# Kernel optimization log

Measured on AMD Instinct MI355X. Metric: run time of the kernel, lower is better.

Reference implementation:

```python
import jax, jax.numpy as jnp
import numpy as np

N_NODES = 20000
N_EDGES = 160000
N_GRAPHS = 64
X_DIM = 9
E_DIM = 1
U_RAW = 4096
U_DIM = 256
E_HID = 1024
E_OUT = 512
N_HID = 512
N_OUT = 1


def _lin_params(k, fan_in, fan_out):
    kw, kb = jax.random.split(k)
    bound = 1.0 / np.sqrt(fan_in)
    W = jax.random.uniform(kw, (fan_in, fan_out), jnp.float32, -bound, bound)
    b = jax.random.uniform(kb, (fan_out,), jnp.float32, -bound, bound)
    return W, b


def setup_inputs() -> dict:
    key = jax.random.key(0)
    ks = jax.random.split(key, 16)
    x = jax.random.normal(ks[0], (N_NODES, X_DIM), jnp.float32)
    edge_attr = jax.random.normal(ks[1], (N_EDGES, E_DIM), jnp.float32)
    u = jax.random.normal(ks[2], (N_GRAPHS, U_RAW), jnp.float32)
    edge_index = jax.random.randint(ks[3], (2, N_EDGES), 0, N_NODES, jnp.int64)
    batch = jax.random.randint(ks[4], (N_NODES,), 0, N_GRAPHS, jnp.int64)

    Wsel, bsel = _lin_params(ks[5], U_RAW, U_DIM)
    e_in = E_DIM + 2 * X_DIM + U_DIM  # 275
    eW1, eb1 = _lin_params(ks[6], e_in, E_HID)
    eW2, eb2 = _lin_params(ks[7], E_HID, E_HID)
    eW3, eb3 = _lin_params(ks[8], E_HID, E_HID)
    eW4, eb4 = _lin_params(ks[9], E_HID, E_HID)
    eW5, eb5 = _lin_params(ks[10], E_HID, E_OUT)
    n1W1, n1b1 = _lin_params(ks[11], E_OUT + X_DIM, N_HID)  # 521
    n1W2, n1b2 = _lin_params(ks[12], N_HID, N_HID)
    n2W1, n2b1 = _lin_params(ks[13], X_DIM + N_HID + U_DIM, N_HID)  # 777
    n2W2, n2b2 = _lin_params(ks[14], N_HID, N_OUT)

    return dict(x=x, edge_attr=edge_attr, u=u, edge_index=edge_index, batch=batch,
                Wsel=Wsel, bsel=bsel,
                eW1=eW1, eb1=eb1, eW2=eW2, eb2=eb2, eW3=eW3, eb3=eb3,
                eW4=eW4, eb4=eb4, eW5=eW5, eb5=eb5,
                n1W1=n1W1, n1b1=n1b1, n1W2=n1W2, n1b2=n1b2,
                n2W1=n2W1, n2b1=n2b1, n2W2=n2W2, n2b2=n2b2)


def _forward(x, edge_attr, u, edge_index, batch,
             Wsel, bsel, eW1, eb1, eW2, eb2, eW3, eb3, eW4, eb4, eW5, eb5,
             n1W1, n1b1, n1W2, n1b2, n2W1, n2b1, n2W2, n2b2):
    relu = jax.nn.relu
    u2 = u @ Wsel + bsel  # [B, 256]
    row, col = edge_index[0], edge_index[1]

    # EdgeModel: cat([src, dest, edge_attr, u[batch[row]]]) -> 5-layer MLP
    e = jnp.concatenate([x[row], x[col], edge_attr, u2[batch[row]]], axis=1)
    e = relu(e @ eW1 + eb1)
    e = relu(e @ eW2 + eb2)
    e = relu(e @ eW3 + eb3)
    e = relu(e @ eW4 + eb4)
    e = e @ eW5 + eb5  # [E, 512]

    # NodeModel: gather x[col], MLP1, scatter_mean over row, MLP2
    h = jnp.concatenate([x[col], e], axis=1)
    h = relu(h @ n1W1 + n1b1)
    h = relu(h @ n1W2 + n1b2)  # [E, 512]
    ssum = jax.ops.segment_sum(h, row, num_segments=x.shape[0])
    cnt = jax.ops.segment_sum(jnp.ones((h.shape[0],), h.dtype), row, num_segments=x.shape[0])
    agg = ssum / jnp.maximum(cnt, 1.0)[:, None]  # scatter_mean

    z = jnp.concatenate([x, agg, u2[batch]], axis=1)
    z = relu(z @ n2W1 + n2b1)
    z = z @ n2W2 + n2b2  # [N, 1]
    return jnp.squeeze(z)


def reference(x, edge_attr, u, edge_index, batch,
              Wsel, bsel, eW1, eb1, eW2, eb2, eW3, eb3, eW4, eb4, eW5, eb5,
              n1W1, n1b1, n1W2, n1b2, n2W1, n2b1, n2W2, n2b2):
    return _forward(x, edge_attr, u, edge_index, batch,
                    Wsel, bsel, eW1, eb1, eW2, eb2, eW3, eb3, eW4, eb4, eW5, eb5,
                    n1W1, n1b1, n1W2, n1b2, n2W1, n2b1, n2W2, n2b2)
```

## Files before the change

kernel.cpp:

```cpp
#include <hip/hip_runtime.h>

typedef _Float16 f16;
typedef __attribute__((ext_vector_type(8))) _Float16 f16x8;
typedef __attribute__((ext_vector_type(4))) float f32x4;

#define E_TOTAL 160000
#define NN 20000
#define NGRAPH 64

__device__ __forceinline__ void gl_lds16(const void* g, void* l) {
    __builtin_amdgcn_global_load_lds((const __attribute__((address_space(1))) void*)g,
                                     (__attribute__((address_space(3))) void*)l, 16, 0, 0);
}

template <int RELU, int AUXU, int AUXX, int SCAT>
__global__ __launch_bounds__(512, 2) void hgemm2(
    int M, int N, int K,
    const f16* __restrict__ A, int lda,
    const f16* __restrict__ Bt,
    f16* __restrict__ C, int ldc,
    const float* __restrict__ bias,
    const f16* __restrict__ utab, const int* __restrict__ uidx,
    const float* __restrict__ x9, const int* __restrict__ xidx, const float* __restrict__ W9,
    float* __restrict__ sout, const int* __restrict__ sidx)
{
    __shared__ __align__(16) char Ash[2][32768];
    __shared__ __align__(16) char Bsh[2][32768];
    __shared__ float Ws9[AUXX ? 2304 : 1];

    const int tid  = threadIdx.x;
    const int lane = tid & 63;
    const int w    = tid >> 6;
    const int bm = blockIdx.y * 256;
    const int bn = blockIdx.x * 256;
    const int wm = (w >> 2) * 128;
    const int wn = (w & 3) * 64;
    const int fr = lane & 15;
    const int kq = lane >> 4;

    const char* Ab = (const char*)A;
    const char* Bb = (const char*)Bt;
    const size_t lda2 = (size_t)lda * 2;
    const size_t ldb2 = (size_t)K * 2;

    f32x4 acc[8][4] = {};

    size_t offA[4], offB[4];
    int ldsoff[4];
#pragma unroll
    for (int i = 0; i < 4; ++i) {
        int cch = w * 4 + i;
        int L = cch * 1024 + lane * 16;
        int row = L >> 7;
        int scb = (L & 127) ^ ((row & 7) << 4);
        offA[i] = (size_t)(bm + row) * lda2 + scb;
        offB[i] = (size_t)(bn + row) * ldb2 + scb;
        ldsoff[i] = cch * 1024;
    }

    const int NT = K >> 6;

#pragma unroll
    for (int i = 0; i < 4; ++i) gl_lds16(Ab + offA[i], Ash[0] + ldsoff[i]);
#pragma unroll
    for (int i = 0; i < 4; ++i) gl_lds16(Bb + offB[i], Bsh[0] + ldsoff[i]);

    int cur = 0;
    for (int t = 0; t < NT; ++t) {
        if (t + 1 < NT) {
            size_t kb = (size_t)(t + 1) << 7;
#pragma unroll
            for (int i = 0; i < 4; ++i) gl_lds16(Ab + offA[i] + kb, Ash[cur ^ 1] + ldsoff[i]);
#pragma unroll
            for (int i = 0; i < 4; ++i) gl_lds16(Bb + offB[i] + kb, Bsh[cur ^ 1] + ldsoff[i]);
            asm volatile("s_waitcnt vmcnt(8)" ::: "memory");
        } else {
            asm volatile("s_waitcnt vmcnt(0)" ::: "memory");
        }
        __builtin_amdgcn_s_barrier();
        __builtin_amdgcn_sched_barrier(0);

        const char* As = Ash[cur];
        const char* Bs = Bsh[cur];

        f16x8 bv[2][4];
#pragma unroll
        for (int ks = 0; ks < 2; ++ks) {
            const int cb = (ks * 32 + kq * 8) * 2;
#pragma unroll
            for (int ni = 0; ni < 4; ++ni) {
                int r = wn + ni * 16 + fr;
                bv[ks][ni] = *(const f16x8*)(Bs + r * 128 + (cb ^ ((r & 7) << 4)));
            }
        }
        __builtin_amdgcn_s_setprio(1);
#pragma unroll
        for (int mi = 0; mi < 8; ++mi) {
            int r = wm + mi * 16 + fr;
            int sw = (r & 7) << 4;
            f16x8 a0 = *(const f16x8*)(As + r * 128 + ((kq * 16) ^ sw));
            f16x8 a1 = *(const f16x8*)(As + r * 128 + ((64 + kq * 16) ^ sw));
#pragma unroll
            for (int ni = 0; ni < 4; ++ni)
                acc[mi][ni] = __builtin_amdgcn_mfma_f32_16x16x32_f16(a0, bv[0][ni], acc[mi][ni], 0, 0, 0);
#pragma unroll
            for (int ni = 0; ni < 4; ++ni)
                acc[mi][ni] = __builtin_amdgcn_mfma_f32_16x16x32_f16(a1, bv[1][ni], acc[mi][ni], 0, 0, 0);
        }
        __builtin_amdgcn_s_setprio(0);
        __builtin_amdgcn_s_barrier();
        cur ^= 1;
    }

    if (AUXX) {
        for (int i = tid; i < 9 * 256; i += 512)
            Ws9[i] = W9[(size_t)(i >> 8) * N + bn + (i & 255)];
        __syncthreads();
    }

#pragma unroll
    for (int mi = 0; mi < 8; ++mi) {
        int r0 = bm + wm + mi * 16 + kq * 4;
#pragma unroll
        for (int r = 0; r < 4; ++r) {
            int grow = r0 + r;
            if (grow >= M) continue;
            int ub = 0;
            if (AUXU) ub = uidx[grow];
            int sb = 0;
            if (SCAT) sb = sidx[grow];
            float xv[9];
            if (AUXX) {
                int xi = xidx ? xidx[grow] : grow;
#pragma unroll
                for (int q = 0; q < 9; ++q) xv[q] = x9[(size_t)xi * 9 + q];
            }
#pragma unroll
            for (int ni = 0; ni < 4; ++ni) {
                int lcol = wn + ni * 16 + fr;
                int col = bn + lcol;
                float v = acc[mi][ni][r] + bias[col];
                if (AUXU) v += (float)utab[(size_t)ub * N + col];
                if (AUXX) {
                    float s = 0.f;
#pragma unroll
                    for (int q = 0; q < 9; ++q) s = fmaf(xv[q], Ws9[q * 256 + lcol], s);
                    v += s;
                }
                if (RELU) v = fmaxf(v, 0.f);
                if (SCAT) {
                    atomicAdd(sout + (size_t)sb * N + col, v);
                } else {
                    C[(size_t)grow * ldc + col] = (f16)v;
                }
            }
        }
    }
}

__global__ void k_wt(const float* __restrict__ W, f16* __restrict__ Wt,
                     int r0, int Ksub, int N, int Kp)
{
    size_t t = (size_t)blockIdx.x * 256 + threadIdx.x;
    if (t >= (size_t)N * Kp) return;
    int n = (int)(t / Kp), k = (int)(t % Kp);
    Wt[t] = (k < Ksub) ? (f16)W[(size_t)(r0 + k) * N + n] : (f16)0.f;
}

__global__ void k_cvt(const float* __restrict__ W, f16* __restrict__ Wt, int n)
{
    int t = blockIdx.x * 256 + threadIdx.x;
    if (t < n) Wt[t] = (f16)W[t];
}

__global__ void k_cbias(const float* __restrict__ n1W1, const float* __restrict__ eb5,
                        const float* __restrict__ n1b1, float* __restrict__ cb)
{
    int b = blockIdx.x * 256 + threadIdx.x;
    if (b >= 512) return;
    float s = n1b1[b];
    for (int c = 0; c < 512; ++c) s = fmaf(eb5[c], n1W1[(size_t)(9 + c) * 512 + b], s);
    cb[b] = s;
}

__global__ __launch_bounds__(256) void k_u2(const float* __restrict__ u,
                                            const float* __restrict__ Wsel,
                                            const float* __restrict__ bsel,
                                            f16* __restrict__ u2h)
{
    __shared__ float us[4096];
    __shared__ float red[4][64];
    const int g = blockIdx.y;
    const int c0 = blockIdx.x * 64;
    const int col = threadIdx.x & 63;
    const int kp = threadIdx.x >> 6;
    for (int i = threadIdx.x; i < 4096; i += 256) us[i] = u[(size_t)g * 4096 + i];
    __syncthreads();
    float acc = 0.f;
    for (int k = kp * 1024; k < kp * 1024 + 1024; ++k)
        acc = fmaf(us[k], Wsel[(size_t)k * 256 + c0 + col], acc);
    red[kp][col] = acc;
    __syncthreads();
    if (kp == 0) {
        float v = red[0][col] + red[1][col] + red[2][col] + red[3][col] + bsel[c0 + col];
        u2h[(size_t)g * 256 + c0 + col] = (f16)v;
    }
}

__global__ void k_gather19(int e0, int Ce,
                           const float* __restrict__ x, const float* __restrict__ eattr,
                           const int* __restrict__ ei, const int* __restrict__ batch,
                           f16* __restrict__ feat, int* __restrict__ ebat)
{
    size_t t = (size_t)blockIdx.x * 256 + threadIdx.x;
    if (t >= (size_t)Ce * 64) return;
    int i = (int)(t >> 6), j = (int)(t & 63);
    int e = e0 + i;
    float v = 0.f;
    if (j < 9)        v = x[ei[e] * 9 + j];
    else if (j < 18)  v = x[ei[E_TOTAL + e] * 9 + (j - 9)];
    else if (j == 18) v = eattr[e];
    else if (j == 19) ebat[i] = batch[ei[e]];
    feat[t] = (f16)v;
}

__global__ void k_cnt(const int* __restrict__ ei, float* __restrict__ cnt)
{
    int t = blockIdx.x * 256 + threadIdx.x;
    if (t < E_TOTAL) atomicAdd(cnt + ei[t], 1.0f);
}

__global__ void k_agg(const float* __restrict__ ssum, const float* __restrict__ cnt,
                      f16* __restrict__ agg)
{
    size_t t = (size_t)blockIdx.x * 256 + threadIdx.x;
    if (t >= (size_t)NN * 512) return;
    int n = (int)(t >> 9);
    agg[t] = (f16)(ssum[t] / fmaxf(cnt[n], 1.f));
}

__global__ void k_final(const f16* __restrict__ z1, const float* __restrict__ W,
                        const float* __restrict__ b, float* __restrict__ out)
{
    int gt = blockIdx.x * 256 + threadIdx.x;
    int row = gt >> 6;
    int lane = threadIdx.x & 63;
    if (row >= NN) return;
    float s = 0.f;
#pragma unroll
    for (int c = lane; c < 512; c += 64) s += (float)z1[(size_t)row * 512 + c] * W[c];
#pragma unroll
    for (int off = 32; off; off >>= 1) s += __shfl_down(s, off);
    if (lane == 0) out[row] = s + b[0];
}


extern "C" void kernel_launch(void* const* d_in, const int* in_sizes, int n_in,
                              void* d_out, int out_size, void* d_ws, size_t ws_size,
                              hipStream_t stream)
{
    const float* x     = (const float*)d_in[0];
    const float* eattr = (const float*)d_in[1];
    const float* u     = (const float*)d_in[2];
    const int*   ei    = (const int*)d_in[3];
    const int*   batch = (const int*)d_in[4];
    const float* Wsel  = (const float*)d_in[5];
    const float* bsel  = (const float*)d_in[6];
    const float* eW1 = (const float*)d_in[7],  * eb1 = (const float*)d_in[8];
    const float* eW2 = (const float*)d_in[9],  * eb2 = (const float*)d_in[10];
    const float* eW3 = (const float*)d_in[11], * eb3 = (const float*)d_in[12];
    const float* eW4 = (const float*)d_in[13], * eb4 = (const float*)d_in[14];
    const float* eW5 = (const float*)d_in[15], * eb5 = (const float*)d_in[16];
    const float* n1W1 = (const float*)d_in[17], * n1b1 = (const float*)d_in[18];
    const float* n1W2 = (const float*)d_in[19], * n1b2 = (const float*)d_in[20];
    const float* n2W1 = (const float*)d_in[21], * n2b1 = (const float*)d_in[22];
    const float* n2W2 = (const float*)d_in[23], * n2b2 = (const float*)d_in[24];
    float* out = (float*)d_out;

    char* ws = (char*)d_ws;
    size_t off = 0;
    auto alc = [&](size_t bytes) { char* p = ws + off; off += (bytes + 255) & ~(size_t)255; return p; };

    float* ssum  = (float*)alc((size_t)NN * 512 * 4);
    float* cnt   = (float*)alc((size_t)NN * 4);
    float* zbias = (float*)alc(1024 * 4);
    float* cbias = (float*)alc(512 * 4);
    f16* u2h     = (f16*)alc((size_t)256 * 256 * 2);
    f16* ubias_e = (f16*)alc((size_t)64 * 1024 * 2);
    f16* ubias_n = (f16*)alc((size_t)64 * 512 * 2);
    f16* eW1t19  = (f16*)alc((size_t)1024 * 64 * 2);
    f16* eW1ut   = (f16*)alc((size_t)1024 * 256 * 2);
    f16* eW2t    = (f16*)alc((size_t)1024 * 1024 * 2);
    f16* eW3t    = (f16*)alc((size_t)1024 * 1024 * 2);
    f16* eW4t    = (f16*)alc((size_t)1024 * 1024 * 2);
    f16* eW5h    = (f16*)alc((size_t)1024 * 512 * 2);
    f16* combo_t = (f16*)alc((size_t)512 * 1024 * 2);
    f16* n1W1et  = (f16*)alc((size_t)512 * 512 * 2);
    f16* n1W2t   = (f16*)alc((size_t)512 * 512 * 2);
    f16* n2W1et  = (f16*)alc((size_t)512 * 512 * 2);
    f16* n2W1ut  = (f16*)alc((size_t)512 * 256 * 2);
    f16* agg     = (f16*)alc((size_t)20224 * 512 * 2);
    f16* z1      = (f16*)alc((size_t)20224 * 512 * 2);
    size_t fixed = off;

    size_t per_edge = 64 * 2 + 1024 * 2 + 1024 * 2 + 4;
    size_t avail = ws_size > fixed ? ws_size - fixed : 0;
    long long Cmax = (long long)(avail / per_edge);
    int C;
    if (Cmax >= E_TOTAL)      C = E_TOTAL;
    else if (Cmax >= 16384)   C = (int)((Cmax / 16384) * 16384);
    else                      C = (int)((Cmax / 256) * 256);
    if (C < 256) C = 256;

    f16* featc = (f16*)(ws + fixed);
    f16* buf1  = featc + (size_t)C * 64;
    f16* buf2  = buf1 + (size_t)C * 1024;
    int* ebat  = (int*)(buf2 + (size_t)C * 1024);

    size_t zlen = (size_t)((char*)zbias - (char*)ssum) + 1024 * 4;
    hipMemsetAsync(ssum, 0, zlen, stream);

    auto wt = [&](const float* W, f16* Wt, int r0, int Ksub, int N, int Kp) {
        size_t tot = (size_t)N * Kp;
        k_wt<<<(unsigned)((tot + 255) / 256), 256, 0, stream>>>(W, Wt, r0, Ksub, N, Kp);
    };
    wt(eW1, eW1t19, 0, 19, 1024, 64);
    wt(eW1, eW1ut, 19, 256, 1024, 256);
    wt(eW2, eW2t, 0, 1024, 1024, 1024);
    wt(eW3, eW3t, 0, 1024, 1024, 1024);
    wt(eW4, eW4t, 0, 1024, 1024, 1024);
    wt(n1W1, n1W1et, 9, 512, 512, 512);
    wt(n1W2, n1W2t, 0, 512, 512, 512);
    wt(n2W1, n2W1et, 9, 512, 512, 512);
    wt(n2W1, n2W1ut, 521, 256, 512, 256);
    k_cvt<<<(1024 * 512 + 255) / 256, 256, 0, stream>>>(eW5, eW5h, 1024 * 512);

    k_u2<<<dim3(4, NGRAPH), 256, 0, stream>>>(u, Wsel, bsel, u2h);
    k_cnt<<<(E_TOTAL + 255) / 256, 256, 0, stream>>>(ei, cnt);
    k_cbias<<<2, 256, 0, stream>>>(n1W1, eb5, n1b1, cbias);

    hgemm2<0,0,0,0><<<dim3(4, 1), 512, 0, stream>>>(64, 1024, 256, u2h, 256, eW1ut,
        ubias_e, 1024, eb1, nullptr, nullptr, nullptr, nullptr, nullptr, nullptr, nullptr);
    hgemm2<0,0,0,0><<<dim3(2, 1), 512, 0, stream>>>(64, 512, 256, u2h, 256, n2W1ut,
        ubias_n, 512, n2b1, nullptr, nullptr, nullptr, nullptr, nullptr, nullptr, nullptr);

    hgemm2<0,0,0,0><<<dim3(4, 2), 512, 0, stream>>>(512, 1024, 512, n1W1et, 512, eW5h,
        combo_t, 1024, zbias, nullptr, nullptr, nullptr, nullptr, nullptr, nullptr, nullptr);

    for (int e0 = 0; e0 < E_TOTAL; e0 += C) {
        int Ce = E_TOTAL - e0 < C ? E_TOTAL - e0 : C;
        int gy = (Ce + 255) / 256;

        k_gather19<<<(unsigned)(((size_t)Ce * 64 + 255) / 256), 256, 0, stream>>>(
            e0, Ce, x, eattr, ei, batch, featc, ebat);

        hgemm2<1,1,0,0><<<dim3(4, gy), 512, 0, stream>>>(Ce, 1024, 64, featc, 64, eW1t19,
            buf1, 1024, zbias, ubias_e, ebat, nullptr, nullptr, nullptr, nullptr, nullptr);
        hgemm2<1,0,0,0><<<dim3(4, gy), 512, 0, stream>>>(Ce, 1024, 1024, buf1, 1024, eW2t,
            buf2, 1024, eb2, nullptr, nullptr, nullptr, nullptr, nullptr, nullptr, nullptr);
        hgemm2<1,0,0,0><<<dim3(4, gy), 512, 0, stream>>>(Ce, 1024, 1024, buf2, 1024, eW3t,
            buf1, 1024, eb3, nullptr, nullptr, nullptr, nullptr, nullptr, nullptr, nullptr);
        hgemm2<1,0,0,0><<<dim3(4, gy), 512, 0, stream>>>(Ce, 1024, 1024, buf1, 1024, eW4t,
            buf2, 1024, eb4, nullptr, nullptr, nullptr, nullptr, nullptr, nullptr, nullptr);

        hgemm2<1,0,1,0><<<dim3(2, gy), 512, 0, stream>>>(Ce, 512, 1024, buf2, 1024, combo_t,
            buf1, 512, cbias, nullptr, nullptr, x, ei + E_TOTAL + e0, n1W1, nullptr, nullptr);

        hgemm2<1,0,0,1><<<dim3(2, gy), 512, 0, stream>>>(Ce, 512, 512, buf1, 512, n1W2t,
            nullptr, 512, n1b2, nullptr, nullptr, nullptr, nullptr, nullptr, ssum, ei + e0);
    }

    k_agg<<<(unsigned)(((size_t)NN * 512 + 255) / 256), 256, 0, stream>>>(ssum, cnt, agg);
    hgemm2<1,1,1,0><<<dim3(2, 79), 512, 0, stream>>>(NN, 512, 512, agg, 512, n2W1et,
        z1, 512, zbias, ubias_n, batch, x, nullptr, n2W1, nullptr, nullptr);
    k_final<<<(NN * 64 + 255) / 256, 256, 0, stream>>>(z1, n2W2, n2b2, out);
}
```

Before: 2.373 ms.

## Split GEMM K-tile into half-tiles with interleaved staged loads and MFMA phases

Restructures the main fp16 GEMM loop so each 64-wide K tile is stored as two 32-wide halves in LDS with a new swizzle, and the loop runs four MFMA phases. Each phase issues part of the next tile's global-to-LDS loads between its LDS reads and its MFMAs, which is meant to spread memory traffic across compute and lower register pressure from the preloaded B fragments. In exchange it adds more barriers per iteration and relies on finer vmcnt accounting.

Result: no change. 2.348 ms (-1.1%).

```diff
diff --git a/kernel.cpp b/kernel.cpp
--- a/kernel.cpp
+++ b/kernel.cpp
@@ -13,8 +13,15 @@
                                      (__attribute__((address_space(3))) void*)l, 16, 0, 0);
 }
 
+#define MFMA16(a, b, c) __builtin_amdgcn_mfma_f32_16x16x32_f16((a), (b), (c), 0, 0, 0)
+#define LGKM0 do { asm volatile("s_waitcnt lgkmcnt(0)" ::: "memory"); \
+                   __builtin_amdgcn_sched_barrier(0); } while (0)
+#define VMW4  asm volatile("s_waitcnt vmcnt(4)" ::: "memory")
+#define VMW0  asm volatile("s_waitcnt vmcnt(0)" ::: "memory")
+#define SBAR  __builtin_amdgcn_s_barrier()
+
 template <int RELU, int AUXU, int AUXX, int SCAT>
-__global__ __launch_bounds__(512, 2) void hgemm2(
+__global__ __launch_bounds__(512, 2) void hgemm8(
     int M, int N, int K,
     const f16* __restrict__ A, int lda,
     const f16* __restrict__ Bt,
@@ -24,8 +31,8 @@
     const float* __restrict__ x9, const int* __restrict__ xidx, const float* __restrict__ W9,
     float* __restrict__ sout, const int* __restrict__ sidx)
 {
-    __shared__ __align__(16) char Ash[2][32768];
-    __shared__ __align__(16) char Bsh[2][32768];
+    __shared__ __align__(16) char Ash[2][2][16384];
+    __shared__ __align__(16) char Bsh[2][2][16384];
     __shared__ float Ws9[AUXX ? 2304 : 1];
 
     const int tid  = threadIdx.x;
@@ -45,71 +52,123 @@
 
     f32x4 acc[8][4] = {};
 
-    size_t offA[4], offB[4];
-    int ldsoff[4];
-#pragma unroll
-    for (int i = 0; i < 4; ++i) {
-        int cch = w * 4 + i;
-        int L = cch * 1024 + lane * 16;
-        int row = L >> 7;
-        int scb = (L & 127) ^ ((row & 7) << 4);
-        offA[i] = (size_t)(bm + row) * lda2 + scb;
-        offB[i] = (size_t)(bn + row) * ldb2 + scb;
-        ldsoff[i] = cch * 1024;
+    int aoff[8], boff[4];
+#pragma unroll
+    for (int mi = 0; mi < 8; ++mi) {
+        int r = wm + mi * 16 + fr;
+        aoff[mi] = r * 64 + ((kq ^ ((r >> 1) & 3)) << 4);
+    }
+#pragma unroll
+    for (int ni = 0; ni < 4; ++ni) {
+        int r = wn + ni * 16 + fr;
+        boff[ni] = r * 64 + ((kq ^ ((r >> 1) & 3)) << 4);
+    }
+
+    int sdest[2];
+    size_t gsrcA[2], gsrcB[2];
+#pragma unroll
+    for (int i = 0; i < 2; ++i) {
+        int L = i * 8192 + tid * 16;
+        int row = L >> 6;
+        int s = (L >> 4) & 3;
+        int sw = (s ^ ((row >> 1) & 3)) << 4;
+        sdest[i] = L;
+        gsrcA[i] = (size_t)(bm + row) * lda2 + sw;
+        gsrcB[i] = (size_t)(bn + row) * ldb2 + sw;
     }
 
     const int NT = K >> 6;
 
-#pragma unroll
-    for (int i = 0; i < 4; ++i) gl_lds16(Ab + offA[i], Ash[0] + ldsoff[i]);
-#pragma unroll
-    for (int i = 0; i < 4; ++i) gl_lds16(Bb + offB[i], Bsh[0] + ldsoff[i]);
-
-    int cur = 0;
+    auto stageA = [&](int t, int h, int buf) {
+        size_t kb = (size_t)t * 128 + h * 64;
+#pragma unroll
+        for (int i = 0; i < 2; ++i)
+            gl_lds16(Ab + gsrcA[i] + kb, &Ash[buf][h][0] + sdest[i]);
+    };
+    auto stageB = [&](int t, int h, int buf) {
+        size_t kb = (size_t)t * 128 + h * 64;
+#pragma unroll
+        for (int i = 0; i < 2; ++i)
+            gl_lds16(Bb + gsrcB[i] + kb, &Bsh[buf][h][0] + sdest[i]);
+    };
+
+    stageA(0, 0, 0); stageB(0, 0, 0); stageA(0, 1, 0); stageB(0, 1, 0);
+    VMW4;
+    SBAR;
+
     for (int t = 0; t < NT; ++t) {
-        if (t + 1 < NT) {
-            size_t kb = (size_t)(t + 1) << 7;
-#pragma unroll
-            for (int i = 0; i < 4; ++i) gl_lds16(Ab + offA[i] + kb, Ash[cur ^ 1] + ldsoff[i]);
-#pragma unroll
-            for (int i = 0; i < 4; ++i) gl_lds16(Bb + offB[i] + kb, Bsh[cur ^ 1] + ldsoff[i]);
-            asm volatile("s_waitcnt vmcnt(8)" ::: "memory");
-        } else {
-            asm volatile("s_waitcnt vmcnt(0)" ::: "memory");
-        }
-        __builtin_amdgcn_s_barrier();
-        __builtin_amdgcn_sched_barrier(0);
-
-        const char* As = Ash[cur];
-        const char* Bs = Bsh[cur];
-
-        f16x8 bv[2][4];
-#pragma unroll
-        for (int ks = 0; ks < 2; ++ks) {
-            const int cb = (ks * 32 + kq * 8) * 2;
-#pragma unroll
-            for (int ni = 0; ni < 4; ++ni) {
-                int r = wn + ni * 16 + fr;
-                bv[ks][ni] = *(const f16x8*)(Bs + r * 128 + (cb ^ ((r & 7) << 4)));
-            }
-        }
+        const int cur = t & 1, nxt = cur ^ 1;
+        const bool pre = (t + 1 < NT);
+        const char* A0 = &Ash[cur][0][0];
+        const char* A1 = &Ash[cur][1][0];
+        const char* B0 = &Bsh[cur][0][0];
+        const char* B1 = &Bsh[cur][1][0];
+
+        f16x8 a0[4], b0[4];
+#pragma unroll
+        for (int i = 0; i < 4; ++i) a0[i] = *(const f16x8*)(A0 + aoff[i]);
+#pragma unroll
+        for (int i = 0; i < 4; ++i) b0[i] = *(const f16x8*)(B0 + boff[i]);
+        if (pre) stageA(t + 1, 0, nxt);
+        SBAR;
+        LGKM0;
         __builtin_amdgcn_s_setprio(1);
 #pragma unroll
-        for (int mi = 0; mi < 8; ++mi) {
-            int r = wm + mi * 16 + fr;
-            int sw = (r & 7) << 4;
-            f16x8 a0 = *(const f16x8*)(As + r * 128 + ((kq * 16) ^ sw));
-            f16x8 a1 = *(const f16x8*)(As + r * 128 + ((64 + kq * 16) ^ sw));
+        for (int mi = 0; mi < 4; ++mi)
 #pragma unroll
             for (int ni = 0; ni < 4; ++ni)
-                acc[mi][ni] = __builtin_amdgcn_mfma_f32_16x16x32_f16(a0, bv[0][ni], acc[mi][ni], 0, 0, 0);
+                acc[mi][ni] = MFMA16(a0[mi], b0[ni], acc[mi][ni]);
+        __builtin_amdgcn_s_setprio(0);
+        SBAR;
+
+        f16x8 a1[4];
+#pragma unroll
+        for (int i = 0; i < 4; ++i) a1[i] = *(const f16x8*)(A0 + aoff[4 + i]);
+        if (pre) stageB(t + 1, 0, nxt);
+        SBAR;
+        LGKM0;
+        __builtin_amdgcn_s_setprio(1);
+#pragma unroll
+        for (int mi = 0; mi < 4; ++mi)
 #pragma unroll
             for (int ni = 0; ni < 4; ++ni)
-                acc[mi][ni] = __builtin_amdgcn_mfma_f32_16x16x32_f16(a1, bv[1][ni], acc[mi][ni], 0, 0, 0);
-        }
+                acc[4 + mi][ni] = MFMA16(a1[mi], b0[ni], acc[4 + mi][ni]);
         __builtin_amdgcn_s_setprio(0);
-        __builtin_amdgcn_s_barrier();
-        cur ^= 1;
+        if (pre) { VMW4; } else { VMW0; }
+        SBAR;
+
+        f16x8 a2[4], b2[4];
+#pragma unroll
+        for (int i = 0; i < 4; ++i) a2[i] = *(const f16x8*)(A1 + aoff[i]);
+#pragma unroll
+        for (int i = 0; i < 4; ++i) b2[i] = *(const f16x8*)(B1 + boff[i]);
+        if (pre) stageA(t + 1, 1, nxt);
+        SBAR;
+        LGKM0;
+        __builtin_amdgcn_s_setprio(1);
+#pragma unroll
+        for (int mi = 0; mi < 4; ++mi)
+#pragma unroll
+            for (int ni = 0; ni < 4; ++ni)
+                acc[mi][ni] = MFMA16(a2[mi], b2[ni], acc[mi][ni]);
+        __builtin_amdgcn_s_setprio(0);
+        SBAR;
+
+        f16x8 a3[4];
+#pragma unroll
+        for (int i = 0; i < 4; ++i) a3[i] = *(const f16x8*)(A1 + aoff[4 + i]);
+        if (pre) stageB(t + 1, 1, nxt);
+        SBAR;
+        LGKM0;
+        __builtin_amdgcn_s_setprio(1);
+#pragma unroll
+        for (int mi = 0; mi < 4; ++mi)
+#pragma unroll
+            for (int ni = 0; ni < 4; ++ni)
+                acc[4 + mi][ni] = MFMA16(a3[mi], b2[ni], acc[4 + mi][ni]);
+        __builtin_amdgcn_s_setprio(0);
+        if (pre) { VMW4; }
+        SBAR;
     }
 
     if (AUXX) {
@@ -339,12 +398,12 @@
     k_cnt<<<(E_TOTAL + 255) / 256, 256, 0, stream>>>(ei, cnt);
     k_cbias<<<2, 256, 0, stream>>>(n1W1, eb5, n1b1, cbias);
 
-    hgemm2<0,0,0,0><<<dim3(4, 1), 512, 0, stream>>>(64, 1024, 256, u2h, 256, eW1ut,
+    hgemm8<0,0,0,0><<<dim3(4, 1), 512, 0, stream>>>(64, 1024, 256, u2h, 256, eW1ut,
         ubias_e, 1024, eb1, nullptr, nullptr, nullptr, nullptr, nullptr, nullptr, nullptr);
-    hgemm2<0,0,0,0><<<dim3(2, 1), 512, 0, stream>>>(64, 512, 256, u2h, 256, n2W1ut,
+    hgemm8<0,0,0,0><<<dim3(2, 1), 512, 0, stream>>>(64, 512, 256, u2h, 256, n2W1ut,
         ubias_n, 512, n2b1, nullptr, nullptr, nullptr, nullptr, nullptr, nullptr, nullptr);
 
-    hgemm2<0,0,0,0><<<dim3(4, 2), 512, 0, stream>>>(512, 1024, 512, n1W1et, 512, eW5h,
+    hgemm8<0,0,0,0><<<dim3(4, 2), 512, 0, stream>>>(512, 1024, 512, n1W1et, 512, eW5h,
         combo_t, 1024, zbias, nullptr, nullptr, nullptr, nullptr, nullptr, nullptr, nullptr);
 
     for (int e0 = 0; e0 < E_TOTAL; e0 += C) {
@@ -354,24 +413,24 @@
         k_gather19<<<(unsigned)(((size_t)Ce * 64 + 255) / 256), 256, 0, stream>>>(
             e0, Ce, x, eattr, ei, batch, featc, ebat);
 
-        hgemm2<1,1,0,0><<<dim3(4, gy), 512, 0, stream>>>(Ce, 1024, 64, featc, 64, eW1t19,
+        hgemm8<1,1,0,0><<<dim3(4, gy), 512, 0, stream>>>(Ce, 1024, 64, featc, 64, eW1t19,
             buf1, 1024, zbias, ubias_e, ebat, nullptr, nullptr, nullptr, nullptr, nullptr);
-        hgemm2<1,0,0,0><<<dim3(4, gy), 512, 0, stream>>>(Ce, 1024, 1024, buf1, 1024, eW2t,
+        hgemm8<1,0,0,0><<<dim3(4, gy), 512, 0, stream>>>(Ce, 1024, 1024, buf1, 1024, eW2t,
             buf2, 1024, eb2, nullptr, nullptr, nullptr, nullptr, nullptr, nullptr, nullptr);
-        hgemm2<1,0,0,0><<<dim3(4, gy), 512, 0, stream>>>(Ce, 1024, 1024, buf2, 1024, eW3t,
+        hgemm8<1,0,0,0><<<dim3(4, gy), 512, 0, stream>>>(Ce, 1024, 1024, buf2, 1024, eW3t,
             buf1, 1024, eb3, nullptr, nullptr, nullptr, nullptr, nullptr, nullptr, nullptr);
-        hgemm2<1,0,0,0><<<dim3(4, gy), 512, 0, stream>>>(Ce, 1024, 1024, buf1, 1024, eW4t,
+        hgemm8<1,0,0,0><<<dim3(4, gy), 512, 0, stream>>>(Ce, 1024, 1024, buf1, 1024, eW4t,
             buf2, 1024, eb4, nullptr, nullptr, nullptr, nullptr, nullptr, nullptr, nullptr);
 
-        hgemm2<1,0,1,0><<<dim3(2, gy), 512, 0, stream>>>(Ce, 512, 1024, buf2, 1024, combo_t,
+        hgemm8<1,0,1,0><<<dim3(2, gy), 512, 0, stream>>>(Ce, 512, 1024, buf2, 1024, combo_t,
             buf1, 512, cbias, nullptr, nullptr, x, ei + E_TOTAL + e0, n1W1, nullptr, nullptr);
 
-        hgemm2<1,0,0,1><<<dim3(2, gy), 512, 0, stream>>>(Ce, 512, 512, buf1, 512, n1W2t,
+        hgemm8<1,0,0,1><<<dim3(2, gy), 512, 0, stream>>>(Ce, 512, 512, buf1, 512, n1W2t,
             nullptr, 512, n1b2, nullptr, nullptr, nullptr, nullptr, nullptr, ssum, ei + e0);
     }
 
     k_agg<<<(unsigned)(((size_t)NN * 512 + 255) / 256), 256, 0, stream>>>(ssum, cnt, agg);
-    hgemm2<1,1,1,0><<<dim3(2, 79), 512, 0, stream>>>(NN, 512, 512, agg, 512, n2W1et,
+    hgemm8<1,1,1,0><<<dim3(2, 79), 512, 0, stream>>>(NN, 512, 512, agg, 512, n2W1et,
         z1, 512, zbias, ubias_n, batch, x, nullptr, n2W1, nullptr, nullptr);
     k_final<<<(NN * 64 + 255) / 256, 256, 0, stream>>>(z1, n2W2, n2b2, out);
 }
```
